# Optimization experiments

Measured on AMD Instinct MI355X. Metric: run time of the kernel, lower is better.

## Reference

```python
import jax, jax.numpy as jnp
import numpy as np

B, T, HID, OUT = 8, 256, 256, 6
DT = 0.1

def setup_inputs() -> dict:
    key = jax.random.key(0)
    ks = jax.random.split(key, 16)
    n = lambda i, shp, s: jax.random.normal(ks[i], shp, jnp.float32) * s
    return {
        "frames": jax.random.normal(ks[0], (B, T, 3, 64, 64), jnp.float32),
        "hidden_state": jnp.zeros((B, HID), jnp.float32),
        "conv1_w": n(1, (32, 3, 3, 3), 0.2), "conv1_b": jnp.zeros((32,), jnp.float32),
        "conv2_w": n(2, (64, 32, 3, 3), 0.1), "conv2_b": jnp.zeros((64,), jnp.float32),
        "conv3_w": n(3, (128, 64, 3, 3), 0.1), "conv3_b": jnp.zeros((128,), jnp.float32),
        "enc_w": n(4, (HID, 128), 0.08), "enc_b": jnp.zeros((HID,), jnp.float32),
        "ltc_wr": n(5, (HID, HID), 0.05), "ltc_wi": n(6, (HID, HID), 0.05),
        "ltc_b": jnp.zeros((HID,), jnp.float32),
        "ltc_tau": jax.random.uniform(ks[7], (HID,), jnp.float32, 0.5, 1.5),
        "ltc_a": n(8, (HID,), 1.0),
        "dec_w1": n(9, (128, HID), 0.08), "dec_b1": jnp.zeros((128,), jnp.float32),
        "dec_w2": n(10, (64, 128), 0.1), "dec_b2": jnp.zeros((64,), jnp.float32),
        "dec_w3": n(11, (OUT, 64), 0.1), "dec_b3": jnp.zeros((OUT,), jnp.float32),
    }

def _conv(x, w, b):
    y = jax.lax.conv_general_dilated(x, w, (2, 2), [(1, 1), (1, 1)],
                                     dimension_numbers=("NCHW", "OIHW", "NCHW"))
    return y + b[None, :, None, None]

def reference(frames, hidden_state, conv1_w, conv1_b, conv2_w, conv2_b, conv3_w, conv3_b,
              enc_w, enc_b, ltc_wr, ltc_wi, ltc_b, ltc_tau, ltc_a,
              dec_w1, dec_b1, dec_w2, dec_b2, dec_w3, dec_b3):
    Bb, Tt = frames.shape[:2]
    x = frames.reshape(Bb * Tt, 3, 64, 64)
    x = jax.nn.relu(_conv(x, conv1_w, conv1_b))   # (BT,32,32,32)
    x = jax.nn.relu(_conv(x, conv2_w, conv2_b))   # (BT,64,16,16)
    x = jax.nn.relu(_conv(x, conv3_w, conv3_b))   # (BT,128,8,8); adaptive pool to (8,8) is identity here
    feats = x.reshape(Bb, Tt, 128, 8, 8).transpose(0, 1, 3, 4, 2).reshape(Bb, Tt, 64, 128)
    node = feats @ enc_w.T + enc_b                # (B,T,64,HID)
    x_seq = node.mean(axis=2).transpose(1, 0, 2)  # (T,B,HID)

    def step(h, x_t):
        # LTC Euler update, dt=0.1, n_steps=1
        f = jnp.tanh(h @ ltc_wr.T + x_t @ ltc_wi.T + ltc_b)
        h_new = h + DT * (-(1.0 / ltc_tau + f) * h + f * ltc_a)
        y = jax.nn.relu(h_new @ dec_w1.T + dec_b1)
        y = jax.nn.relu(y @ dec_w2.T + dec_b2)
        c = y @ dec_w3.T + dec_b3
        return h_new, c

    final_hidden, controls = jax.lax.scan(step, hidden_state, x_seq)
    return controls.transpose(1, 0, 2), final_hidden
```

## Files before the change

### kernel.cpp

```cpp
#include <hip/hip_runtime.h>

#define T_STEPS 256
#define B_SZ 8
#define HID 256

typedef _Float16 hv2 __attribute__((ext_vector_type(2)));
typedef _Float16 f16x4 __attribute__((ext_vector_type(4)));
typedef float f32x4 __attribute__((ext_vector_type(4)));
union H2U { hv2 h; unsigned u; };
union U2F { uint2 u; f16x4 h; };
__device__ inline hv2 u2h(unsigned u){ H2U c; c.u = u; return c.h; }
__device__ inline unsigned h2u(hv2 h){ H2U c; c.h = h; return c.u; }
__device__ inline hv2 relu2(hv2 v){
  unsigned u = h2u(v);
  unsigned s = (u & 0x80008000u) >> 15;
  u &= ~(s * 0xFFFFu);
  return u2h(u);
}
__device__ inline unsigned packh2f(float lo, float hi){
  hv2 h; h.x = (_Float16)lo; h.y = (_Float16)hi; return h2u(h);
}

#define OFF_XW   0
#define OFF_HH   524288
#define OFF_WFT  1141760
#define OFF_BF   1174528
#define OFF_D1T  1174784
#define OFF_D2T  1207552
#define OFF_D3T  1215744
#define OFF_W1P  1216128
#define OFF_W2F  1216560
#define OFF_W3F  1225776
#define OFF_WRP  1262640

__global__ __launch_bounds__(256) void prep_kernel(
    const float* __restrict__ conv1_w, const float* __restrict__ conv2_w,
    const float* __restrict__ conv3_w, const float* __restrict__ enc_w,
    const float* __restrict__ enc_b,  const float* __restrict__ ltc_wi,
    const float* __restrict__ ltc_b,  const float* __restrict__ ltc_wr,
    const float* __restrict__ dec_w1,
    const float* __restrict__ dec_w2, const float* __restrict__ dec_w3,
    float* __restrict__ ws)
{
  int gtid = blockIdx.x * 256 + threadIdx.x;
  int nth = gridDim.x * 256;
  unsigned* wsu = (unsigned*)ws;
  for (int e = gtid; e < 128 * 256; e += nth) {
    int j = e >> 7, m = e & 127;
    float s = 0.f;
    for (int k = 0; k < 256; ++k) s = fmaf(ltc_wi[j*256 + k], enc_w[k*128 + m], s);
    ws[OFF_WFT + m*256 + j] = s;
  }
  for (int e = gtid; e < 256; e += nth) {
    float s = ltc_b[e];
    for (int k = 0; k < 256; ++k) s = fmaf(ltc_wi[e*256 + k], enc_b[k], s);
    ws[OFF_BF + e] = s;
  }
  for (int e = gtid; e < 27*16; e += nth) { int k = e>>4, p = e&15;
    wsu[OFF_W1P+e] = packh2f(conv1_w[(2*p)*27 + k], conv1_w[(2*p+1)*27 + k]); }
  for (int e = gtid; e < 9216; e += nth) {
    int dpair = e & 1;
    int tmp = e >> 1;
    int l = tmp & 63; tmp >>= 6;
    int nt = tmp & 3; tmp >>= 2;
    int kt = tmp % 9, hp = tmp / 9;
    int oc = nt*16 + (l & 15);
    int ic = hp*16 + ((l>>4)<<2) + (dpair<<1);
    int ky = kt/3, kx = kt%3;
    wsu[OFF_W2F + e] = packh2f(conv2_w[((oc*32 + ic)*3 + ky)*3 + kx],
                               conv2_w[((oc*32 + ic+1)*3 + ky)*3 + kx]);
  }
  for (int e = gtid; e < 36864; e += nth) {
    int dpair = e & 1;
    int tmp = e >> 1;
    int l = tmp & 63; tmp >>= 6;
    int nt = tmp & 7; tmp >>= 3;
    int kt = tmp;
    int kyx = kt >> 2;
    int ky = kyx/3, kx = kyx%3;
    int ic = ((kt & 3) << 4) + ((l>>4)<<2) + (dpair<<1);
    int oc = nt*16 + (l & 15);
    wsu[OFF_W3F + e] = packh2f(conv3_w[((oc*64 + ic)*3 + ky)*3 + kx],
                               conv3_w[((oc*64 + ic+1)*3 + ky)*3 + kx]);
  }
  for (int e = gtid; e < 32768; e += nth) {
    int i = e & 31;
    int j = (e >> 5) & 255;
    int q = e >> 13;
    wsu[OFF_WRP + e] = packh2f(ltc_wr[j*256 + q*64 + 2*i],
                               ltc_wr[j*256 + q*64 + 2*i + 1]);
  }
  for (int e = gtid; e < 256*128;e += nth) { int k = e>>7, i = e&127; ws[OFF_D1T+e] = dec_w1[i*256 + k]; }
  for (int e = gtid; e < 128*64; e += nth) { int k = e>>6, i = e&63;  ws[OFF_D2T+e] = dec_w2[i*128 + k]; }
  for (int e = gtid; e < 64*6;   e += nth) { int k = e/6,  o = e%6;   ws[OFF_D3T+e] = dec_w3[o*64 + k]; }
}

__global__ __launch_bounds__(256, 2) void enc_kernel(
    const float* __restrict__ frames,
    const float* __restrict__ b1, const float* __restrict__ b2,
    const float* __restrict__ b3, float* __restrict__ ws)
{
  extern __shared__ __align__(16) unsigned lds[];
  unsigned* actA = lds;
  unsigned* wst  = lds + 8192;
  unsigned* w1s  = lds + 17408;
  float* fmp = (float*)(lds + 17840);

  const int tid = threadIdx.x;
  const int l   = tid & 63;
  const int w   = tid >> 6;
  const int kg  = l >> 4;
  const int lc  = l & 15;
  const int bt  = blockIdx.x;
  const int b   = bt >> 8, t = bt & 255;
  const float* fr = frames + (size_t)bt * 12288;
  const unsigned* wsu = (const unsigned*)ws;

  {
    const uint4* src = (const uint4*)(wsu + OFF_W2F);
    uint4 tmp[9];
    #pragma unroll
    for (int q = 0; q < 9; ++q) tmp[q] = src[q*256 + tid];
    #pragma unroll
    for (int q = 0; q < 9; ++q) ((uint4*)wst)[q*256 + tid] = tmp[q];
    if (tid < 216) ((uint2*)w1s)[tid] = ((const uint2*)(wsu + OFF_W1P))[tid];
  }
  __syncthreads();

  f32x4 acc2[4][4];
  #pragma unroll
  for (int mi = 0; mi < 4; ++mi)
    #pragma unroll
    for (int nt = 0; nt < 4; ++nt) {
      float bb = b2[nt*16 + lc];
      acc2[mi][nt] = (f32x4){bb, bb, bb, bb};
    }

  for (int hp = 0; hp < 2; ++hp) {
    for (int p = 0; p < 4; ++p) {
      int pos = p*256 + tid;
      int y = pos >> 5, x = pos & 31;
      hv2 a1[8];
      #pragma unroll
      for (int o = 0; o < 8; ++o) { a1[o].x = (_Float16)b1[16*hp+2*o]; a1[o].y = (_Float16)b1[16*hp+2*o+1]; }
      for (int ic = 0; ic < 3; ++ic)
        for (int ky = 0; ky < 3; ++ky) {
          int iy = 2*y - 1 + ky;
          bool rok = (unsigned)iy < 64u;
          for (int kx = 0; kx < 3; ++kx) {
            int ix = 2*x - 1 + kx;
            float v = (rok && (unsigned)ix < 64u) ? fr[ic*4096 + iy*64 + ix] : 0.f;
            _Float16 hf = (_Float16)v;
            hv2 vs; vs.x = hf; vs.y = hf;
            int k = ic*9 + ky*3 + kx;
            uint4 wa = ((uint4*)w1s)[k*4 + hp*2];
            uint4 wb = ((uint4*)w1s)[k*4 + hp*2 + 1];
            a1[0] = vs * u2h(wa.x) + a1[0];
            a1[1] = vs * u2h(wa.y) + a1[1];
            a1[2] = vs * u2h(wa.z) + a1[2];
            a1[3] = vs * u2h(wa.w) + a1[3];
            a1[4] = vs * u2h(wb.x) + a1[4];
            a1[5] = vs * u2h(wb.y) + a1[5];
            a1[6] = vs * u2h(wb.z) + a1[6];
            a1[7] = vs * u2h(wb.w) + a1[7];
          }
        }
      unsigned r0 = h2u(relu2(a1[0])), r1 = h2u(relu2(a1[1]));
      unsigned r2 = h2u(relu2(a1[2])), r3 = h2u(relu2(a1[3]));
      unsigned r4 = h2u(relu2(a1[4])), r5 = h2u(relu2(a1[5]));
      unsigned r6 = h2u(relu2(a1[6])), r7 = h2u(relu2(a1[7]));
      int s = pos & 3;
      uint4 v0, v1;
      if (s & 1) { v0 = make_uint4(r2,r3,r0,r1); v1 = make_uint4(r6,r7,r4,r5); }
      else       { v0 = make_uint4(r0,r1,r2,r3); v1 = make_uint4(r4,r5,r6,r7); }
      int sl = (s >> 1) & 1;
      ((uint4*)actA)[pos*2 + sl]     = v0;
      ((uint4*)actA)[pos*2 + (1^sl)] = v1;
    }
    __syncthreads();
    #pragma unroll
    for (int ky = 0; ky < 3; ++ky)
      #pragma unroll
      for (int kx = 0; kx < 3; ++kx) {
        int kt = ky*3 + kx;
        U2F bf[4];
        #pragma unroll
        for (int nt = 0; nt < 4; ++nt)
          bf[nt].u = ((const uint2*)wst)[(((hp*9 + kt)*4 + nt)<<6) + l];
        #pragma unroll
        for (int mi = 0; mi < 4; ++mi) {
          int mt = w*4 + mi;
          int iy = 2*mt - 1 + ky;
          if (iy >= 0) {
            int ix = 2*lc - 1 + kx;
            bool okx = (unsigned)ix < 32u;
            int pos1 = iy*32 + (okx ? ix : 0);
            U2F av; av.u = ((const uint2*)actA)[pos1*4 + (kg ^ (pos1 & 3))];
            if (!okx) { av.u.x = 0u; av.u.y = 0u; }
            #pragma unroll
            for (int nt = 0; nt < 4; ++nt)
              acc2[mi][nt] = __builtin_amdgcn_mfma_f32_16x16x16f16(av.h, bf[nt].h, acc2[mi][nt], 0, 0, 0);
          }
        }
      }
    __syncthreads();
  }

  {
    const uint4* w3src = (const uint4*)(wsu + OFF_W3F);
    uint4 st[4];
    #pragma unroll
    for (int q = 0; q < 4; ++q) st[q] = w3src[q*256 + tid];
    _Float16* act2h = (_Float16*)wst;
    #pragma unroll
    for (int mi = 0; mi < 4; ++mi)
      #pragma unroll
      for (int nt = 0; nt < 4; ++nt)
        #pragma unroll
        for (int i = 0; i < 4; ++i) {
          int pos = (w*4 + mi)*16 + 4*kg + i;
          int oc = nt*16 + lc;
          float vv = fmaxf(acc2[mi][nt][i], 0.f);
          int ocp = (((oc >> 2) ^ (pos & 7)) << 2) + (oc & 3);
          act2h[pos*64 + ocp] = (_Float16)vv;
        }
    #pragma unroll
    for (int q = 0; q < 4; ++q) ((uint4*)actA)[q*256 + tid] = st[q];
  }

  f32x4 acc3[8];
  #pragma unroll
  for (int nt = 0; nt < 8; ++nt) { float bb = b3[nt*16 + lc]; acc3[nt] = (f32x4){bb, bb, bb, bb}; }
  const int y3 = (w*16 + lc) >> 3, x3 = lc & 7;
  const uint4* w3src = (const uint4*)(wsu + OFF_W3F);
  __syncthreads();

  for (int c = 0; c < 9; ++c) {
    uint4 st[4];
    if (c < 8) {
      #pragma unroll
      for (int q = 0; q < 4; ++q) st[q] = w3src[(c+1)*1024 + q*256 + tid];
    }
    int ky = c / 3, kx = c % 3;
    int iy = 2*y3 - 1 + ky, ix = 2*x3 - 1 + kx;
    bool ok = ((unsigned)iy < 16u) && ((unsigned)ix < 16u);
    int posIn = (ok ? iy : 0)*16 + (ok ? ix : 0);
    int sw = posIn & 7;
    #pragma unroll
    for (int ktl = 0; ktl < 4; ++ktl) {
      int icb = ktl*4 + kg;
      U2F av; av.u = ((const uint2*)wst)[posIn*16 + (icb ^ sw)];
      if (!ok) { av.u.x = 0u; av.u.y = 0u; }
      #pragma unroll
      for (int nt = 0; nt < 8; ++nt) {
        U2F bv; bv.u = ((const uint2*)actA)[(c & 1)*2048 + ((ktl*8 + nt)<<6) + l];
        acc3[nt] = __builtin_amdgcn_mfma_f32_16x16x16f16(av.h, bv.h, acc3[nt], 0, 0, 0);
      }
    }
    if (c < 8) {
      #pragma unroll
      for (int q = 0; q < 4; ++q) ((uint4*)actA)[((c+1) & 1)*1024 + q*256 + tid] = st[q];
    }
    __syncthreads();
  }

  #pragma unroll
  for (int nt = 0; nt < 8; ++nt) {
    float s = 0.f;
    #pragma unroll
    for (int i = 0; i < 4; ++i) s += fmaxf(acc3[nt][i], 0.f);
    s += __shfl_xor(s, 16);
    s += __shfl_xor(s, 32);
    if (l < 16) fmp[w*128 + nt*16 + l] = s;
  }
  __syncthreads();
  if (tid < 128) {
    float s = fmp[tid] + fmp[128 + tid] + fmp[256 + tid] + fmp[384 + tid];
    fmp[tid] = s * (1.f/64.f);
  }
  __syncthreads();
  {
    float accx = ws[OFF_BF + tid];
    const float* wfT = ws + OFF_WFT;
    for (int m = 0; m < 128; ++m) accx = fmaf(fmp[m], wfT[m*256 + tid], accx);
    ws[OFF_XW + (t*B_SZ + b)*HID + tid] = accx;
  }
}

__global__ __launch_bounds__(1024) void scan_kernel(
    const float* __restrict__ tau, const float* __restrict__ av,
    const float* __restrict__ h0,
    float* __restrict__ ws, float* __restrict__ outh)
{
  const int b = blockIdx.x;
  const int tid = threadIdx.x;
  const int j = tid & 255, q = tid >> 8;
  __shared__ float hf[256];
  __shared__ unsigned hp16[128];
  __shared__ float part[4][256];
  __shared__ float hbuf[16*256];

  uint4 wv[8];
  {
    const uint4* wp = (const uint4*)((const unsigned*)ws + OFF_WRP + (q*256 + j)*32);
    #pragma unroll
    for (int r = 0; r < 8; ++r) wv[r] = wp[r];
  }
  const float tinv = 1.f / tau[j];
  const float aj = av[j];
  const float* xw = ws + OFF_XW;
  float* hh = ws + OFF_HH;

  {
    float hv0 = h0[b*256 + j];
    float hvn = __shfl_xor(hv0, 1);
    if (q == 0) {
      hf[j] = hv0;
      if (!(j & 1)) hp16[j >> 1] = packh2f(hv0, hvn);
    }
  }
  float xw_pref = xw[(0*B_SZ + b)*HID + j];
  __syncthreads();

  for (int t = 0; t < T_STEPS; ++t) {
    float xwv = xw_pref;
    xw_pref = xw[((t+1)*B_SZ + b)*HID + j];
    hv2 acc = {(_Float16)0.f, (_Float16)0.f};
    const uint4* hq = (const uint4*)hp16 + q*8;
    #pragma unroll
    for (int r = 0; r < 8; ++r) {
      uint4 hvp = hq[r];
      acc = u2h(hvp.x) * u2h(wv[r].x) + acc;
      acc = u2h(hvp.y) * u2h(wv[r].y) + acc;
      acc = u2h(hvp.z) * u2h(wv[r].z) + acc;
      acc = u2h(hvp.w) * u2h(wv[r].w) + acc;
    }
    float hv0 = hf[j];
    part[q][j] = (float)acc.x + (float)acc.y;
    __syncthreads();
    float pre = part[0][j] + part[1][j] + part[2][j] + part[3][j] + xwv;
    float f = 1.f - 2.f / (1.f + __expf(2.f * pre));
    float hn = fmaf(0.1f, fmaf(-(tinv + f), hv0, f * aj), hv0);
    float hnn = __shfl_xor(hn, 1);
    if (q == 0) {
      hf[j] = hn;
      hbuf[(t & 15)*256 + j] = hn;
      if (!(j & 1)) hp16[j >> 1] = packh2f(hn, hnn);
    }
    __syncthreads();
    if ((t & 15) == 15) {
      int base = t - 15;
      int st = tid >> 6;
      int col = (tid & 63) << 2;
      *(float4*)(hh + ((base + st)*B_SZ + b)*HID + col) = *(float4*)(hbuf + st*256 + col);
    }
  }
  if (q == 0) outh[b*HID + j] = hf[j];
}

__global__ __launch_bounds__(256) void dec_kernel(
    const float* __restrict__ db1, const float* __restrict__ db2,
    const float* __restrict__ db3, const float* __restrict__ ws,
    float* __restrict__ outc)
{
  const int bid = blockIdx.x;
  const int b = bid >> 8, t = bid & 255;
  const int tid = threadIdx.x;
  __shared__ float hloc[256];
  __shared__ float p1[2][128];
  __shared__ float y1s[128];
  __shared__ float p2[4][64];
  __shared__ float y2s[64];
  const float* hh  = ws + OFF_HH + (t*B_SZ + b)*HID;
  const float* d1T = ws + OFF_D1T;
  const float* d2T = ws + OFF_D2T;
  const float* d3T = ws + OFF_D3T;
  hloc[tid] = hh[tid];
  __syncthreads();
  {
    int i = tid & 127, hf = tid >> 7;
    float s = 0.f;
    for (int k = hf*128; k < hf*128 + 128; ++k) s = fmaf(hloc[k], d1T[k*128 + i], s);
    p1[hf][i] = s;
  }
  __syncthreads();
  if (tid < 128) y1s[tid] = fmaxf(p1[0][tid] + p1[1][tid] + db1[tid], 0.f);
  __syncthreads();
  {
    int i = tid & 63, r = tid >> 6;
    float s = 0.f;
    for (int k = r*32; k < r*32 + 32; ++k) s = fmaf(y1s[k], d2T[k*64 + i], s);
    p2[r][i] = s;
  }
  __syncthreads();
  if (tid < 64) y2s[tid] = fmaxf(p2[0][tid] + p2[1][tid] + p2[2][tid] + p2[3][tid] + db2[tid], 0.f);
  __syncthreads();
  if (tid < 6) {
    float s = db3[tid];
    for (int k = 0; k < 64; ++k) s = fmaf(y2s[k], d3T[k*6 + tid], s);
    outc[(b*T_STEPS + t)*6 + tid] = s;
  }
}

extern "C" void kernel_launch(void* const* d_in, const int* in_sizes, int n_in,
                              void* d_out, int out_size, void* d_ws, size_t ws_size,
                              hipStream_t stream)
{
  const float* frames = (const float*)d_in[0];
  const float* h0   = (const float*)d_in[1];
  const float* c1w  = (const float*)d_in[2];
  const float* c1b  = (const float*)d_in[3];
  const float* c2w  = (const float*)d_in[4];
  const float* c2b  = (const float*)d_in[5];
  const float* c3w  = (const float*)d_in[6];
  const float* c3b  = (const float*)d_in[7];
  const float* encw = (const float*)d_in[8];
  const float* encb = (const float*)d_in[9];
  const float* wr   = (const float*)d_in[10];
  const float* wi   = (const float*)d_in[11];
  const float* lb   = (const float*)d_in[12];
  const float* ltau = (const float*)d_in[13];
  const float* la   = (const float*)d_in[14];
  const float* dw1  = (const float*)d_in[15];
  const float* db1  = (const float*)d_in[16];
  const float* dw2  = (const float*)d_in[17];
  const float* db2  = (const float*)d_in[18];
  const float* dw3  = (const float*)d_in[19];
  const float* db3  = (const float*)d_in[20];
  float* out = (float*)d_out;
  float* ws  = (float*)d_ws;

  hipLaunchKernelGGL(prep_kernel, dim3(256), dim3(256), 0, stream,
                     c1w, c2w, c3w, encw, encb, wi, lb, wr, dw1, dw2, dw3, ws);
  hipLaunchKernelGGL(enc_kernel, dim3(2048), dim3(256), 73408, stream,
                     frames, c1b, c2b, c3b, ws);
  hipLaunchKernelGGL(scan_kernel, dim3(B_SZ), dim3(1024), 0, stream,
                     ltau, la, h0, ws, out + 12288);
  hipLaunchKernelGGL(dec_kernel, dim3(2048), dim3(256), 0, stream,
                     db1, db2, db3, ws, out);
}
```

Before: 488.0 us.

## Cut encoder LDS footprint to fit three blocks per CU

The encoder no longer stages conv2 weights in LDS; it reads them straight from global memory (through cache) during the conv2 MFMA loop. The conv3 weight double buffer is split into 18 half-size chunks instead of 9, which shrinks LDS use from about 73KB to about 53KB. Launch bounds are raised to 3 blocks per CU. The aim is higher occupancy to hide latency, at the cost of global or L2 loads in the conv2 inner loop, twice as many barriers in conv3, and tighter register limits.

```diff
diff --git a/kernel.cpp b/kernel.cpp
--- a/kernel.cpp
+++ b/kernel.cpp
@@ -95,16 +95,16 @@
   for (int e = gtid; e < 64*6;   e += nth) { int k = e/6,  o = e%6;   ws[OFF_D3T+e] = dec_w3[o*64 + k]; }
 }
 
-__global__ __launch_bounds__(256, 2) void enc_kernel(
+__global__ __launch_bounds__(256, 3) void enc_kernel(
     const float* __restrict__ frames,
     const float* __restrict__ b1, const float* __restrict__ b2,
     const float* __restrict__ b3, float* __restrict__ ws)
 {
   extern __shared__ __align__(16) unsigned lds[];
-  unsigned* actA = lds;
-  unsigned* wst  = lds + 8192;
-  unsigned* w1s  = lds + 17408;
-  float* fmp = (float*)(lds + 17840);
+  unsigned* buf0  = lds;
+  unsigned* w3buf = lds + 8192;
+  unsigned* w1s   = lds + 12288;
+  float* fmp = (float*)(lds + 12720);
 
   const int tid = threadIdx.x;
   const int l   = tid & 63;
@@ -115,16 +115,10 @@
   const int b   = bt >> 8, t = bt & 255;
   const float* fr = frames + (size_t)bt * 12288;
   const unsigned* wsu = (const unsigned*)ws;
-
-  {
-    const uint4* src = (const uint4*)(wsu + OFF_W2F);
-    uint4 tmp[9];
-    #pragma unroll
-    for (int q = 0; q < 9; ++q) tmp[q] = src[q*256 + tid];
-    #pragma unroll
-    for (int q = 0; q < 9; ++q) ((uint4*)wst)[q*256 + tid] = tmp[q];
-    if (tid < 216) ((uint2*)w1s)[tid] = ((const uint2*)(wsu + OFF_W1P))[tid];
-  }
+  const uint2* w2f = (const uint2*)(wsu + OFF_W2F);
+  const uint4* w3src = (const uint4*)(wsu + OFF_W3F);
+
+  if (tid < 216) ((uint2*)w1s)[tid] = ((const uint2*)(wsu + OFF_W1P))[tid];
   __syncthreads();
 
   f32x4 acc2[4][4];
@@ -174,8 +168,8 @@
       if (s & 1) { v0 = make_uint4(r2,r3,r0,r1); v1 = make_uint4(r6,r7,r4,r5); }
       else       { v0 = make_uint4(r0,r1,r2,r3); v1 = make_uint4(r4,r5,r6,r7); }
       int sl = (s >> 1) & 1;
-      ((uint4*)actA)[pos*2 + sl]     = v0;
-      ((uint4*)actA)[pos*2 + (1^sl)] = v1;
+      ((uint4*)buf0)[pos*2 + sl]     = v0;
+      ((uint4*)buf0)[pos*2 + (1^sl)] = v1;
     }
     __syncthreads();
     #pragma unroll
@@ -186,7 +180,7 @@
         U2F bf[4];
         #pragma unroll
         for (int nt = 0; nt < 4; ++nt)
-          bf[nt].u = ((const uint2*)wst)[(((hp*9 + kt)*4 + nt)<<6) + l];
+          bf[nt].u = w2f[(((hp*9 + kt)*4 + nt)<<6) + l];
         #pragma unroll
         for (int mi = 0; mi < 4; ++mi) {
           int mt = w*4 + mi;
@@ -195,7 +189,7 @@
             int ix = 2*lc - 1 + kx;
             bool okx = (unsigned)ix < 32u;
             int pos1 = iy*32 + (okx ? ix : 0);
-            U2F av; av.u = ((const uint2*)actA)[pos1*4 + (kg ^ (pos1 & 3))];
+            U2F av; av.u = ((const uint2*)buf0)[pos1*4 + (kg ^ (pos1 & 3))];
             if (!okx) { av.u.x = 0u; av.u.y = 0u; }
             #pragma unroll
             for (int nt = 0; nt < 4; ++nt)
@@ -207,11 +201,9 @@
   }
 
   {
-    const uint4* w3src = (const uint4*)(wsu + OFF_W3F);
-    uint4 st[4];
-    #pragma unroll
-    for (int q = 0; q < 4; ++q) st[q] = w3src[q*256 + tid];
-    _Float16* act2h = (_Float16*)wst;
+    uint4 s0a = w3src[tid];
+    uint4 s0b = w3src[256 + tid];
+    _Float16* act2h = (_Float16*)buf0;
     #pragma unroll
     for (int mi = 0; mi < 4; ++mi)
       #pragma unroll
@@ -224,42 +216,44 @@
           int ocp = (((oc >> 2) ^ (pos & 7)) << 2) + (oc & 3);
           act2h[pos*64 + ocp] = (_Float16)vv;
         }
-    #pragma unroll
-    for (int q = 0; q < 4; ++q) ((uint4*)actA)[q*256 + tid] = st[q];
+    ((uint4*)w3buf)[tid] = s0a;
+    ((uint4*)w3buf)[256 + tid] = s0b;
   }
 
   f32x4 acc3[8];
   #pragma unroll
   for (int nt = 0; nt < 8; ++nt) { float bb = b3[nt*16 + lc]; acc3[nt] = (f32x4){bb, bb, bb, bb}; }
   const int y3 = (w*16 + lc) >> 3, x3 = lc & 7;
-  const uint4* w3src = (const uint4*)(wsu + OFF_W3F);
-  __syncthreads();
-
-  for (int c = 0; c < 9; ++c) {
-    uint4 st[4];
-    if (c < 8) {
-      #pragma unroll
-      for (int q = 0; q < 4; ++q) st[q] = w3src[(c+1)*1024 + q*256 + tid];
-    }
-    int ky = c / 3, kx = c % 3;
+  __syncthreads();
+
+  for (int cc = 0; cc < 18; ++cc) {
+    uint4 st0, st1;
+    if (cc < 17) {
+      st0 = w3src[(cc+1)*512 + tid];
+      st1 = w3src[(cc+1)*512 + 256 + tid];
+    }
+    int kyx = cc >> 1;
+    int ky = kyx / 3, kx = kyx % 3;
     int iy = 2*y3 - 1 + ky, ix = 2*x3 - 1 + kx;
     bool ok = ((unsigned)iy < 16u) && ((unsigned)ix < 16u);
     int posIn = (ok ? iy : 0)*16 + (ok ? ix : 0);
     int sw = posIn & 7;
-    #pragma unroll
-    for (int ktl = 0; ktl < 4; ++ktl) {
-      int icb = ktl*4 + kg;
-      U2F av; av.u = ((const uint2*)wst)[posIn*16 + (icb ^ sw)];
+    const uint2* bvp = (const uint2*)w3buf + (cc & 1)*1024;
+    #pragma unroll
+    for (int k2 = 0; k2 < 2; ++k2) {
+      int kt = 2*cc + k2;
+      int icb = (kt & 3)*4 + kg;
+      U2F av; av.u = ((const uint2*)buf0)[posIn*16 + (icb ^ sw)];
       if (!ok) { av.u.x = 0u; av.u.y = 0u; }
       #pragma unroll
       for (int nt = 0; nt < 8; ++nt) {
-        U2F bv; bv.u = ((const uint2*)actA)[(c & 1)*2048 + ((ktl*8 + nt)<<6) + l];
+        U2F bv; bv.u = bvp[((k2*8 + nt)<<6) + l];
         acc3[nt] = __builtin_amdgcn_mfma_f32_16x16x16f16(av.h, bv.h, acc3[nt], 0, 0, 0);
       }
     }
-    if (c < 8) {
-      #pragma unroll
-      for (int q = 0; q < 4; ++q) ((uint4*)actA)[((c+1) & 1)*1024 + q*256 + tid] = st[q];
+    if (cc < 17) {
+      ((uint4*)w3buf)[((cc+1)&1)*512 + tid] = st0;
+      ((uint4*)w3buf)[((cc+1)&1)*512 + 256 + tid] = st1;
     }
     __syncthreads();
   }
@@ -432,7 +426,7 @@
 
   hipLaunchKernelGGL(prep_kernel, dim3(256), dim3(256), 0, stream,
                      c1w, c2w, c3w, encw, encb, wi, lb, wr, dw1, dw2, dw3, ws);
-  hipLaunchKernelGGL(enc_kernel, dim3(2048), dim3(256), 73408, stream,
+  hipLaunchKernelGGL(enc_kernel, dim3(2048), dim3(256), 52928, stream,
                      frames, c1b, c2b, c3b, ws);
   hipLaunchKernelGGL(scan_kernel, dim3(B_SZ), dim3(1024), 0, stream,
                      ltau, la, h0, ws, out + 12288);
```

New measurement: 503.2 us. 3.1% more time.
